# Performance work log

Hardware: AMD Instinct MI355X
Metric: run time of the kernel (lower is better)

The kernel has to match this reference:

```python
import jax, jax.numpy as jnp
import numpy as np

H = 4096        # hidden_size
NH = 32         # num query heads
NG = 8          # num query groups (kv heads)
HD = H // NH    # head size = 128
B, S = 2, 2048


def gen_rope_cache(seq_length, n_elem, base=10000.0):
    theta = 1.0 / base ** (jnp.arange(0, n_elem, 2, dtype=jnp.float32) / n_elem)
    idx_theta = jnp.outer(jnp.arange(seq_length, dtype=jnp.float32), theta)
    return jnp.stack([jnp.cos(idx_theta), jnp.sin(idx_theta)], axis=-1)  # [S, n_elem//2, 2]


def apply_rope(x, cache):
    # x: [B, S, nh, hd], cache: [S, hd//2, 2]; rot_dim == hd (no pass-through)
    b, s, nh, hd = x.shape
    xr = x.reshape(b, s, nh, hd // 2, 2)
    c = cache[:s].reshape(1, s, 1, hd // 2, 2)
    out = jnp.stack([
        xr[..., 0] * c[..., 0] - xr[..., 1] * c[..., 1],
        xr[..., 1] * c[..., 0] + xr[..., 0] * c[..., 1],
    ], axis=-1)
    return out.reshape(b, s, nh, hd)


def setup_inputs() -> dict:
    key = jax.random.key(0)
    k1, k2, k3, k4 = jax.random.split(key, 4)
    x = jax.random.normal(k1, (B, S, H), dtype=jnp.float32)
    W_qkv = jax.random.normal(k2, (H, H + 2 * NG * HD), dtype=jnp.float32) * 0.02
    b_qkv = jax.random.normal(k3, (H + 2 * NG * HD,), dtype=jnp.float32) * 0.02
    W_dense = jax.random.normal(k4, (H, H), dtype=jnp.float32) * 0.02
    rope_cache = gen_rope_cache(S, HD)
    return {"x": x, "rope_cache": rope_cache, "W_qkv": W_qkv, "b_qkv": b_qkv, "W_dense": W_dense}


def reference(x, rope_cache, W_qkv, b_qkv, W_dense):
    b, s, h = x.shape
    qkv = jnp.einsum('bsh,ho->bso', x, W_qkv) + b_qkv
    q, k, v = jnp.split(qkv, [h, h + NG * HD], axis=-1)
    q = q.reshape(b, s, NH, HD)
    k = k.reshape(b, s, NG, HD)
    v = v.reshape(b, s, NG, HD)
    q = apply_rope(q, rope_cache)
    k = apply_rope(k, rope_cache)
    # GQA: group query heads [B, G, rep, S, D] against kv [B, G, S, D]
    rep = NH // NG
    qg = q.transpose(0, 2, 1, 3).reshape(b, NG, rep, s, HD)
    kg = k.transpose(0, 2, 1, 3)  # [B, G, S, D]
    vg = v.transpose(0, 2, 1, 3)
    scale = 1.0 / jnp.sqrt(jnp.float32(HD))
    scores = jnp.einsum('bgrqd,bgkd->bgrqk', qg, kg) * scale
    causal = jnp.tril(jnp.ones((s, s), dtype=bool))
    scores = jnp.where(causal, scores, jnp.float32(-1e30))
    attn = jax.nn.softmax(scores, axis=-1)
    out = jnp.einsum('bgrqk,bgkd->bgrqd', attn, vg)  # [B, G, rep, S, D]
    out = out.reshape(b, NH, s, HD).transpose(0, 2, 1, 3).reshape(b, s, h)
    return jnp.einsum('bsh,ho->bso', out, W_dense)
```

## Files before the change

### kernel.cpp

```cpp
#include <hip/hip_runtime.h>
#include <hip/hip_bf16.h>
#include <math.h>

#define BS   4096
#define HH   4096
#define NH   32
#define NG   8
#define HD   128
#define SEQ  2048
#define NQKV 6144

typedef float f32x4 __attribute__((ext_vector_type(4)));
typedef float f32x16 __attribute__((ext_vector_type(16)));
typedef short s16x8 __attribute__((ext_vector_type(8)));
typedef short s16x4 __attribute__((ext_vector_type(4)));
typedef unsigned int u32x4 __attribute__((ext_vector_type(4)));

__device__ __forceinline__ unsigned short f2bf(float f) {
  unsigned int u = __builtin_bit_cast(unsigned int, f);
  unsigned int r = (u + 0x7fffu + ((u >> 16) & 1u)) >> 16;
  return (unsigned short)r;
}
__device__ __forceinline__ float b2f(short h) {
  unsigned int u = ((unsigned int)(unsigned short)h) << 16;
  return __builtin_bit_cast(float, u);
}

__device__ __forceinline__ void gload16(const void* g, void* l) {
  __builtin_amdgcn_global_load_lds((__attribute__((address_space(1))) void*)(g),
                                   (__attribute__((address_space(3))) void*)(l), 16, 0, 0);
}

#define BARRIER __builtin_amdgcn_s_barrier()
#define PRIO1 __builtin_amdgcn_s_setprio(1)
#define PRIO0 __builtin_amdgcn_s_setprio(0)

__global__ void cast_f32_bf16(const float* __restrict__ in, short* __restrict__ out, long n4) {
  long i = (long)blockIdx.x * blockDim.x + threadIdx.x;
  long stride = (long)gridDim.x * blockDim.x;
  for (; i < n4; i += stride) {
    float4 v = *(const float4*)&in[i * 4];
    s16x4 o;
    o[0] = (short)f2bf(v.x); o[1] = (short)f2bf(v.y);
    o[2] = (short)f2bf(v.z); o[3] = (short)f2bf(v.w);
    *(s16x4*)&out[i * 4] = o;
  }
}

__global__ __launch_bounds__(256) void transpose_cast(const float* __restrict__ in,
                                                      short* __restrict__ out, int R, int C) {
  __shared__ float tile[32][33];
  int tx = threadIdx.x & 31, ty = threadIdx.x >> 5;
  long c0 = (long)blockIdx.x * 32, r0 = (long)blockIdx.y * 32;
#pragma unroll
  for (int j = 0; j < 32; j += 8)
    tile[ty + j][tx] = in[(r0 + ty + j) * C + c0 + tx];
  __syncthreads();
#pragma unroll
  for (int j = 0; j < 32; j += 8)
    out[(c0 + ty + j) * R + r0 + tx] = (short)f2bf(tile[tx][ty + j]);
}

#define LDA_FR(BASE, DB)                                                         \
  {                                                                              \
    _Pragma("unroll") for (int mf = 0; mf < 4; ++mf)                             \
      _Pragma("unroll") for (int ks = 0; ks < 2; ++ks)                           \
        af[mf][ks] = *(const s16x8*)&lds[(BASE) + (DB) * 8192 + aoff[mf][ks]];   \
  }
#define LDB_FR(BASE, DB)                                                         \
  {                                                                              \
    _Pragma("unroll") for (int nf = 0; nf < 2; ++nf)                             \
      _Pragma("unroll") for (int ks = 0; ks < 2; ++ks)                           \
        bf[nf][ks] = *(const s16x8*)&lds[(BASE) + (DB) * 8192 + boff[nf][ks]];   \
  }
#define MF_Q(MS, NS)                                                             \
  {                                                                              \
    _Pragma("unroll") for (int ks = 0; ks < 2; ++ks)                             \
      _Pragma("unroll") for (int mf = 0; mf < 4; ++mf)                           \
        _Pragma("unroll") for (int nf = 0; nf < 2; ++nf)                         \
          acc[(MS) * 4 + mf][(NS) * 2 + nf] = __builtin_amdgcn_mfma_f32_16x16x32_bf16( \
              af[mf][ks], bf[nf][ks], acc[(MS) * 4 + mf][(NS) * 2 + nf], 0, 0, 0);     \
  }
#define STG_AU0(DB, KB) { gload16(sA0 + (KB), &lds[0 + (DB) * 8192 + du0]);            \
                          gload16(sA1 + (KB), &lds[0 + (DB) * 8192 + du1]); }
#define STG_BU0(DB, KB) { gload16(sB0 + (KB), &lds[32768 + (DB) * 8192 + du0]);        \
                          gload16(sB1 + (KB), &lds[32768 + (DB) * 8192 + du1]); }
#define STG_AU1(DB, KB) { gload16(sA0 + 64 * (long)K + (KB), &lds[16384 + (DB) * 8192 + du0]); \
                          gload16(sA1 + 64 * (long)K + (KB), &lds[16384 + (DB) * 8192 + du1]); }
#define STG_BU1(DB, KB) { gload16(sB0 + 32 * (long)K + (KB), &lds[49152 + (DB) * 8192 + du0]); \
                          gload16(sB1 + 32 * (long)K + (KB), &lds[49152 + (DB) * 8192 + du1]); }

#define TILE256(DB, KBS)                                                         \
  LDA_FR(0, DB); LDB_FR(32768, DB);                                              \
  STG_AU0(DB ^ 1, KBS); STG_BU0(DB ^ 1, KBS);                                    \
  BARRIER;                                                                       \
  PRIO1; MF_Q(0, 0); PRIO0;                                                      \
  asm volatile("s_waitcnt vmcnt(6)" ::: "memory");                               \
  BARRIER;                                                                       \
  LDB_FR(49152, DB);                                                             \
  STG_BU1(DB ^ 1, KBS);                                                          \
  BARRIER;                                                                       \
  PRIO1; MF_Q(0, 1); PRIO0;                                                      \
  asm volatile("s_waitcnt vmcnt(6)" ::: "memory");                               \
  BARRIER;                                                                       \
  LDA_FR(16384, DB);                                                             \
  STG_AU1(DB ^ 1, KBS);                                                          \
  BARRIER;                                                                       \
  PRIO1; MF_Q(1, 1); PRIO0;                                                      \
  BARRIER;                                                                       \
  LDB_FR(32768, DB);                                                             \
  BARRIER;                                                                       \
  PRIO1; MF_Q(1, 0); PRIO0;                                                      \
  asm volatile("s_waitcnt vmcnt(4)" ::: "memory");                               \
  BARRIER;

template <int MODE>
__global__ __launch_bounds__(512, 1) void gemm256(const short* __restrict__ A,
                                                  const short* __restrict__ Bt,
                                                  const float* __restrict__ bias,
                                                  void* __restrict__ Cout,
                                                  const float* __restrict__ cache,
                                                  short* __restrict__ Qb,
                                                  short* __restrict__ Kb,
                                                  short* __restrict__ Vtb,
                                                  int M, int N, int K) {
  extern __shared__ short lds[];
  const int t = threadIdx.x;
  const int lane = t & 63, w = t >> 6;
  const int g = lane >> 4, lr = lane & 15;
  const int wm = w >> 2, wn = w & 3;
  const long bm = (long)blockIdx.y * 256;
  const long bn = (long)blockIdx.x * 256;

  const short *sA0, *sA1, *sB0, *sB1;
  {
    int c0 = t, c1 = t + 512;
    int h0 = c0 >> 9, r0 = (c0 >> 3) & 63, tc0 = (c0 & 7) ^ (r0 & 7);
    int h1 = c1 >> 9, r1 = (c1 >> 3) & 63, tc1 = (c1 & 7) ^ (r1 & 7);
    sA0 = A + (bm + h0 * 128 + r0) * (long)K + tc0 * 8;
    sA1 = A + (bm + h1 * 128 + r1) * (long)K + tc1 * 8;
    int g0 = c0 >> 8, rb0 = (c0 >> 3) & 31, tb0 = (c0 & 7) ^ (rb0 & 7);
    int g1 = c1 >> 8, rb1 = (c1 >> 3) & 31, tb1 = (c1 & 7) ^ (rb1 & 7);
    sB0 = Bt + (bn + g0 * 64 + rb0) * (long)K + tb0 * 8;
    sB1 = Bt + (bn + g1 * 64 + rb1) * (long)K + tb1 * 8;
  }
  const int du0 = w * 512;
  const int du1 = w * 512 + 4096;

  int aoff[4][2], boff[2][2];
#pragma unroll
  for (int mf = 0; mf < 4; ++mf)
#pragma unroll
    for (int ks = 0; ks < 2; ++ks)
      aoff[mf][ks] = wm * 4096 + (mf * 16 + lr) * 64 + (((ks * 4 + g) ^ (lr & 7)) * 8);
#pragma unroll
  for (int nf = 0; nf < 2; ++nf)
#pragma unroll
    for (int ks = 0; ks < 2; ++ks)
      boff[nf][ks] = wn * 2048 + (nf * 16 + lr) * 64 + (((ks * 4 + g) ^ (lr & 7)) * 8);

  f32x4 acc[8][4] = {};
  s16x8 af[4][2], bf[2][2];

  STG_AU0(0, 0); STG_BU0(0, 0); STG_AU1(0, 0); STG_BU1(0, 0);
  asm volatile("s_waitcnt vmcnt(0)" ::: "memory");
  BARRIER;

  const int NT = K >> 6;
  for (int kt = 0; kt < NT; kt += 2) {
    const long kb1 = (long)(kt + 1) * 64;
    const long kb2 = (kt + 2 < NT) ? (long)(kt + 2) * 64 : 0l;
    TILE256(0, kb1);
    TILE256(1, kb2);
  }

  if (MODE == 0) {
#pragma unroll
    for (int am = 0; am < 8; ++am) {
      long row = bm + wm * 128 + am * 16 + g * 4;
#pragma unroll
      for (int an = 0; an < 4; ++an) {
        long col = bn + wn * 64 + an * 16 + lr;
#pragma unroll
        for (int r = 0; r < 4; ++r)
          ((float*)Cout)[(row + r) * N + col] = acc[am][an][r];
      }
    }
  } else {
    const float scq = 0.12751743f;
#pragma unroll
    for (int am = 0; am < 8; ++am) {
      int row0 = (int)bm + wm * 128 + am * 16 + g * 4;
      int s0 = row0 & (SEQ - 1);
      int bb = row0 >> 11;
#pragma unroll
      for (int an = 0; an < 4; ++an) {
        int col = (int)bn + wn * 64 + an * 16 + lr;
        float bv = bias[col];
        if (col < HH) {
          int h = col >> 7, d = col & 127;
          const int odd = lr & 1;
#pragma unroll
          for (int r = 0; r < 4; ++r) {
            float v = acc[am][an][r] + bv;
            float p = __shfl_xor(v, 1);
            float2 cs = *(const float2*)&cache[((long)(s0 + r) * 64 + (d >> 1)) * 2];
            float o = odd ? (v * cs.x + p * cs.y) : (v * cs.x - p * cs.y);
            Qb[((long)(bb * NH + h) * SEQ + s0 + r) * HD + d] = (short)f2bf(o * scq);
          }
        } else if (col < HH + NG * HD) {
          int cc = col - HH;
          int gi = cc >> 7, d = cc & 127;
          const int odd = lr & 1;
#pragma unroll
          for (int r = 0; r < 4; ++r) {
            float v = acc[am][an][r] + bv;
            float p = __shfl_xor(v, 1);
            float2 cs = *(const float2*)&cache[((long)(s0 + r) * 64 + (d >> 1)) * 2];
            float o = odd ? (v * cs.x + p * cs.y) : (v * cs.x - p * cs.y);
            Kb[((long)(bb * NG + gi) * SEQ + s0 + r) * HD + d] = (short)f2bf(o);
          }
        } else {
          int cc = col - HH - NG * HD;
          int gi = cc >> 7, d = cc & 127;
          s16x4 o;
#pragma unroll
          for (int r = 0; r < 4; ++r) o[r] = (short)f2bf(acc[am][an][r] + bv);
          *(s16x4*)&Vtb[((long)(bb * NG + gi) * HD + d) * SEQ + s0] = o;
        }
      }
    }
  }
}

__global__ __launch_bounds__(512, 1) void attn(const short* __restrict__ Qb,
                                               const short* __restrict__ Kb,
                                               const short* __restrict__ Vtb,
                                               short* __restrict__ Ob) {
  extern __shared__ short alds[];
  const int t = threadIdx.x, lane = t & 63, w = t >> 6;
  const int l31 = lane & 31, hi = lane >> 5;
  const int qt = 7 - (int)(blockIdx.x >> 6);
  const int head = blockIdx.x & 63;
  const int b = head >> 5, h = head & 31;
  const int qb = qt * 256;
  const short* Qhead = Qb + (long)(b * NH + h) * SEQ * HD;
  const short* Khead = Kb + (long)(b * NG + (h >> 2)) * SEQ * HD;
  const short* Vthead = Vtb + (long)(b * NG + (h >> 2)) * SEQ * HD;
  const int qw0 = qb + w * 32;
  const int qrow = qw0 + l31;
  float* facs = (float*)&alds[32768] + w * 32;

  s16x8 qf[8];
#pragma unroll
  for (int ds = 0; ds < 8; ++ds)
    qf[ds] = *(const s16x8*)&Qhead[(long)qrow * HD + ds * 16 + hi * 8];

  const short *kp0, *kp1, *vp0, *vp1;
  {
    int c0 = t, c1 = t + 512;
    int kr0 = c0 >> 4, kc0 = (c0 & 15) ^ (kr0 & 15);
    int kr1 = c1 >> 4, kc1 = (c1 & 15) ^ (kr1 & 15);
    kp0 = Khead + (long)kr0 * HD + kc0 * 8;
    kp1 = Khead + (long)kr1 * HD + kc1 * 8;
    int vr0 = c0 >> 3, vc0 = (c0 & 7) ^ (vr0 & 7);
    int vr1 = c1 >> 3, vc1 = (c1 & 7) ^ (vr1 & 7);
    vp0 = Vthead + (long)vr0 * SEQ + vc0 * 8;
    vp1 = Vthead + (long)vr1 * SEQ + vc1 * 8;
  }
  const int d0 = w * 512, d1 = w * 512 + 4096;

  f32x16 ao[4] = {};
  float mrun = -1.0e30f, lrun = 0.0f;
  const int nkt = 4 * qt + 4;

  gload16(kp0, &alds[d0]); gload16(kp1, &alds[d1]);
  gload16(vp0, &alds[16384 + d0]); gload16(vp1, &alds[16384 + d1]);
  kp0 += 64 * HD; kp1 += 64 * HD; vp0 += 64; vp1 += 64;
  asm volatile("s_waitcnt vmcnt(0)" ::: "memory");
  BARRIER;

  for (int kt = 0; kt < nkt; ++kt) {
    const int buf = kt & 1, nb = buf ^ 1;
    const int kb = kt * 64;
    const int bK = buf * 8192, bV = 16384 + buf * 8192;
    if (kt + 1 < nkt) {
      gload16(kp0, &alds[nb * 8192 + d0]); gload16(kp1, &alds[nb * 8192 + d1]);
      gload16(vp0, &alds[16384 + nb * 8192 + d0]); gload16(vp1, &alds[16384 + nb * 8192 + d1]);
      kp0 += 64 * HD; kp1 += 64 * HD; vp0 += 64; vp1 += 64;
    }
    if (kb <= qw0 + 31) {
      f32x16 st0 = {}, st1 = {};
      PRIO1;
#pragma unroll
      for (int ds = 0; ds < 8; ++ds) {
        const int c = ds * 2 + hi;
        const int r0 = l31, r1 = 32 + l31;
        s16x8 kf0 = *(const s16x8*)&alds[bK + r0 * 128 + ((c ^ (r0 & 15)) * 8)];
        s16x8 kf1 = *(const s16x8*)&alds[bK + r1 * 128 + ((c ^ (r1 & 15)) * 8)];
        st0 = __builtin_amdgcn_mfma_f32_32x32x16_bf16(kf0, qf[ds], st0, 0, 0, 0);
        st1 = __builtin_amdgcn_mfma_f32_32x32x16_bf16(kf1, qf[ds], st1, 0, 0, 0);
      }
      PRIO0;

      float p[32];
      if (kb + 63 > qrow || kb + 63 > qw0) {
#pragma unroll
        for (int r = 0; r < 16; ++r) {
          int kg = kb + (r & 3) + 8 * (r >> 2) + 4 * hi;
          p[r] = (kg > qrow) ? -1.0e30f : st0[r];
          p[16 + r] = (kg + 32 > qrow) ? -1.0e30f : st1[r];
        }
      } else {
#pragma unroll
        for (int r = 0; r < 16; ++r) { p[r] = st0[r]; p[16 + r] = st1[r]; }
      }
      float tmax = -1.0e30f;
#pragma unroll
      for (int i = 0; i < 32; ++i) tmax = fmaxf(tmax, p[i]);
      tmax = fmaxf(tmax, __shfl_xor(tmax, 32));
      if (!__all(tmax <= mrun + 8.0f)) {
        float mnew = fmaxf(mrun, tmax);
        float fac = exp2f(mrun - mnew);
        facs[l31] = fac;
        mrun = mnew; lrun *= fac;
        f32x4 f0 = *(f32x4*)&facs[0 + 4 * hi];
        f32x4 f1 = *(f32x4*)&facs[8 + 4 * hi];
        f32x4 f2 = *(f32x4*)&facs[16 + 4 * hi];
        f32x4 f3 = *(f32x4*)&facs[24 + 4 * hi];
#pragma unroll
        for (int j = 0; j < 4; ++j)
#pragma unroll
          for (int dt = 0; dt < 4; ++dt) {
            ao[dt][j] *= f0[j]; ao[dt][4 + j] *= f1[j];
            ao[dt][8 + j] *= f2[j]; ao[dt][12 + j] *= f3[j];
          }
      }
      float tsum = 0.0f;
#pragma unroll
      for (int i = 0; i < 32; ++i) { p[i] = exp2f(p[i] - mrun); tsum += p[i]; }
      lrun += tsum + __shfl_xor(tsum, 32);

      s16x8 pa[4];
#pragma unroll
      for (int ks = 0; ks < 4; ++ks) {
        unsigned w0, w1, w2, w3;
        asm("v_cvt_pk_bf16_f32 %0, %1, %2" : "=v"(w0) : "v"(p[ks * 8 + 0]), "v"(p[ks * 8 + 1]));
        asm("v_cvt_pk_bf16_f32 %0, %1, %2" : "=v"(w1) : "v"(p[ks * 8 + 2]), "v"(p[ks * 8 + 3]));
        asm("v_cvt_pk_bf16_f32 %0, %1, %2" : "=v"(w2) : "v"(p[ks * 8 + 4]), "v"(p[ks * 8 + 5]));
        asm("v_cvt_pk_bf16_f32 %0, %1, %2" : "=v"(w3) : "v"(p[ks * 8 + 6]), "v"(p[ks * 8 + 7]));
        unsigned sw0 = (unsigned)__shfl_xor((int)w0, 32);
        unsigned sw1 = (unsigned)__shfl_xor((int)w1, 32);
        unsigned sw2 = (unsigned)__shfl_xor((int)w2, 32);
        unsigned sw3 = (unsigned)__shfl_xor((int)w3, 32);
        u32x4 pw;
        pw[0] = hi ? sw2 : w0;
        pw[1] = hi ? sw3 : w1;
        pw[2] = hi ? w2 : sw0;
        pw[3] = hi ? w3 : sw1;
        pa[ks] = __builtin_bit_cast(s16x8, pw);
      }

      PRIO1;
#pragma unroll
      for (int ks = 0; ks < 4; ++ks)
#pragma unroll
        for (int dt = 0; dt < 4; ++dt) {
          int dd = dt * 32 + l31;
          int slot = (ks * 2 + hi) ^ (dd & 7);
          s16x8 vf = *(const s16x8*)&alds[bV + dd * 64 + slot * 8];
          ao[dt] = __builtin_amdgcn_mfma_f32_32x32x16_bf16(pa[ks], vf, ao[dt], 0, 0, 0);
        }
      PRIO0;
    }
    asm volatile("s_waitcnt vmcnt(0)" ::: "memory");
    BARRIER;
  }

  facs[l31] = 1.0f / lrun;
  float invr[16];
  {
    f32x4 i0 = *(f32x4*)&facs[0 + 4 * hi];
    f32x4 i1 = *(f32x4*)&facs[8 + 4 * hi];
    f32x4 i2 = *(f32x4*)&facs[16 + 4 * hi];
    f32x4 i3 = *(f32x4*)&facs[24 + 4 * hi];
#pragma unroll
    for (int j = 0; j < 4; ++j) {
      invr[j] = i0[j]; invr[4 + j] = i1[j]; invr[8 + j] = i2[j]; invr[12 + j] = i3[j];
    }
  }
#pragma unroll
  for (int dt = 0; dt < 4; ++dt)
#pragma unroll
    for (int r = 0; r < 16; ++r) {
      int grow = qw0 + (r & 3) + 8 * (r >> 2) + 4 * hi;
      Ob[((long)b * SEQ + grow) * HH + h * HD + dt * 32 + l31] = (short)f2bf(ao[dt][r] * invr[r]);
    }
}

extern "C" void kernel_launch(void* const* d_in, const int* in_sizes, int n_in,
                              void* d_out, int out_size, void* d_ws, size_t ws_size,
                              hipStream_t stream) {
  const float* x     = (const float*)d_in[0];
  const float* cache = (const float*)d_in[1];
  const float* Wqkv  = (const float*)d_in[2];
  const float* bqkv  = (const float*)d_in[3];
  const float* Wd    = (const float*)d_in[4];

  char* ws = (char*)d_ws;
  short* xb   = (short*)(ws);
  short* wqt  = (short*)(ws + 33554432ll);
  short* wdt  = (short*)(ws + 83886080ll);
  short* Qb   = (short*)(ws + 167772160ll);
  short* Kb   = (short*)(ws + 201326592ll);
  short* Vtb  = (short*)(ws + 218103808ll);
  short* Ob   = (short*)(ws + 226492416ll);

  cast_f32_bf16<<<2048, 256, 0, stream>>>(x, xb, (long)BS * HH / 4);
  transpose_cast<<<dim3(NQKV / 32, HH / 32), 256, 0, stream>>>(Wqkv, wqt, HH, NQKV);
  transpose_cast<<<dim3(HH / 32, HH / 32), 256, 0, stream>>>(Wd, wdt, HH, HH);
  gemm256<2><<<dim3(NQKV / 256, BS / 256), 512, 131072, stream>>>(
      xb, wqt, bqkv, nullptr, cache, Qb, Kb, Vtb, BS, NQKV, HH);
  attn<<<512, 512, 66560, stream>>>(Qb, Kb, Vtb, Ob);
  gemm256<0><<<dim3(HH / 256, BS / 256), 512, 131072, stream>>>(
      Ob, wdt, nullptr, d_out, nullptr, nullptr, nullptr, nullptr, BS, HH, HH);
}
```

Before: 517.4 us.

## Reorder GEMM inner tile by k-substep with smaller register fragments

```diff
diff --git a/kernel.cpp b/kernel.cpp
--- a/kernel.cpp
+++ b/kernel.cpp
@@ -61,26 +61,18 @@
     out[(c0 + ty + j) * R + r0 + tx] = (short)f2bf(tile[tx][ty + j]);
 }
 
-#define LDA_FR(BASE, DB)                                                         \
-  {                                                                              \
-    _Pragma("unroll") for (int mf = 0; mf < 4; ++mf)                             \
-      _Pragma("unroll") for (int ks = 0; ks < 2; ++ks)                           \
-        af[mf][ks] = *(const s16x8*)&lds[(BASE) + (DB) * 8192 + aoff[mf][ks]];   \
-  }
-#define LDB_FR(BASE, DB)                                                         \
-  {                                                                              \
-    _Pragma("unroll") for (int nf = 0; nf < 2; ++nf)                             \
-      _Pragma("unroll") for (int ks = 0; ks < 2; ++ks)                           \
-        bf[nf][ks] = *(const s16x8*)&lds[(BASE) + (DB) * 8192 + boff[nf][ks]];   \
-  }
-#define MF_Q(MS, NS)                                                             \
-  {                                                                              \
-    _Pragma("unroll") for (int ks = 0; ks < 2; ++ks)                             \
-      _Pragma("unroll") for (int mf = 0; mf < 4; ++mf)                           \
-        _Pragma("unroll") for (int nf = 0; nf < 2; ++nf)                         \
-          acc[(MS) * 4 + mf][(NS) * 2 + nf] = __builtin_amdgcn_mfma_f32_16x16x32_bf16( \
-              af[mf][ks], bf[nf][ks], acc[(MS) * 4 + mf][(NS) * 2 + nf], 0, 0, 0);     \
-  }
+#define LDA4(MSB, DB, KS)                                                        \
+  { _Pragma("unroll") for (int mf = 0; mf < 4; ++mf)                             \
+      af4[mf] = *(const s16x8*)&lds[(MSB) + (DB) * 8192 + aoff[mf][KS]]; }
+#define LDB4(DB, KS)                                                             \
+  { _Pragma("unroll") for (int nf = 0; nf < 2; ++nf) {                           \
+      bfr[nf] = *(const s16x8*)&lds[32768 + (DB) * 8192 + boff[nf][KS]];         \
+      bfr[2 + nf] = *(const s16x8*)&lds[49152 + (DB) * 8192 + boff[nf][KS]]; } }
+#define MF_P(MS)                                                                 \
+  { _Pragma("unroll") for (int mf = 0; mf < 4; ++mf)                             \
+      _Pragma("unroll") for (int j = 0; j < 4; ++j)                              \
+        acc[(MS) * 4 + mf][j] = __builtin_amdgcn_mfma_f32_16x16x32_bf16(         \
+            af4[mf], bfr[j], acc[(MS) * 4 + mf][j], 0, 0, 0); }
 #define STG_AU0(DB, KB) { gload16(sA0 + (KB), &lds[0 + (DB) * 8192 + du0]);            \
                           gload16(sA1 + (KB), &lds[0 + (DB) * 8192 + du1]); }
 #define STG_BU0(DB, KB) { gload16(sB0 + (KB), &lds[32768 + (DB) * 8192 + du0]);        \
@@ -91,27 +83,25 @@
                           gload16(sB1 + 32 * (long)K + (KB), &lds[49152 + (DB) * 8192 + du1]); }
 
 #define TILE256(DB, KBS)                                                         \
-  LDA_FR(0, DB); LDB_FR(32768, DB);                                              \
-  STG_AU0(DB ^ 1, KBS); STG_BU0(DB ^ 1, KBS);                                    \
-  BARRIER;                                                                       \
-  PRIO1; MF_Q(0, 0); PRIO0;                                                      \
+  LDA4(0, DB, 0); LDB4(DB, 0);                                                   \
+  STG_AU0(DB ^ 1, KBS); STG_BU0(DB ^ 1, KBS); STG_BU1(DB ^ 1, KBS);              \
+  BARRIER;                                                                       \
+  PRIO1; MF_P(0); PRIO0;                                                         \
   asm volatile("s_waitcnt vmcnt(6)" ::: "memory");                               \
   BARRIER;                                                                       \
-  LDB_FR(49152, DB);                                                             \
-  STG_BU1(DB ^ 1, KBS);                                                          \
-  BARRIER;                                                                       \
-  PRIO1; MF_Q(0, 1); PRIO0;                                                      \
-  asm volatile("s_waitcnt vmcnt(6)" ::: "memory");                               \
-  BARRIER;                                                                       \
-  LDA_FR(16384, DB);                                                             \
+  LDA4(16384, DB, 0);                                                            \
   STG_AU1(DB ^ 1, KBS);                                                          \
   BARRIER;                                                                       \
-  PRIO1; MF_Q(1, 1); PRIO0;                                                      \
-  BARRIER;                                                                       \
-  LDB_FR(32768, DB);                                                             \
-  BARRIER;                                                                       \
-  PRIO1; MF_Q(1, 0); PRIO0;                                                      \
-  asm volatile("s_waitcnt vmcnt(4)" ::: "memory");                               \
+  PRIO1; MF_P(1); PRIO0;                                                         \
+  BARRIER;                                                                       \
+  LDA4(16384, DB, 1); LDB4(DB, 1);                                               \
+  BARRIER;                                                                       \
+  PRIO1; MF_P(1); PRIO0;                                                         \
+  BARRIER;                                                                       \
+  LDA4(0, DB, 1);                                                                \
+  BARRIER;                                                                       \
+  PRIO1; MF_P(0); PRIO0;                                                         \
+  asm volatile("s_waitcnt vmcnt(2)" ::: "memory");                               \
   BARRIER;
 
 template <int MODE>
@@ -160,7 +150,7 @@
       boff[nf][ks] = wn * 2048 + (nf * 16 + lr) * 64 + (((ks * 4 + g) ^ (lr & 7)) * 8);
 
   f32x4 acc[8][4] = {};
-  s16x8 af[4][2], bf[2][2];
+  s16x8 af4[4], bfr[4];
 
   STG_AU0(0, 0); STG_BU0(0, 0); STG_AU1(0, 0); STG_BU1(0, 0);
   asm volatile("s_waitcnt vmcnt(0)" ::: "memory");
```

Result: slower. 529.8 us (+2.4%).

## Split QKV GEMM into separate Q and KV kernels to balance CU waves

Applied to the files above, without the earlier changes.

```diff
diff --git a/kernel.cpp b/kernel.cpp
--- a/kernel.cpp
+++ b/kernel.cpp
@@ -121,8 +121,6 @@
                                                   void* __restrict__ Cout,
                                                   const float* __restrict__ cache,
                                                   short* __restrict__ Qb,
-                                                  short* __restrict__ Kb,
-                                                  short* __restrict__ Vtb,
                                                   int M, int N, int K) {
   extern __shared__ short lds[];
   const int t = threadIdx.x;
@@ -197,37 +195,144 @@
       for (int an = 0; an < 4; ++an) {
         int col = (int)bn + wn * 64 + an * 16 + lr;
         float bv = bias[col];
-        if (col < HH) {
-          int h = col >> 7, d = col & 127;
-          const int odd = lr & 1;
-#pragma unroll
-          for (int r = 0; r < 4; ++r) {
-            float v = acc[am][an][r] + bv;
-            float p = __shfl_xor(v, 1);
-            float2 cs = *(const float2*)&cache[((long)(s0 + r) * 64 + (d >> 1)) * 2];
-            float o = odd ? (v * cs.x + p * cs.y) : (v * cs.x - p * cs.y);
-            Qb[((long)(bb * NH + h) * SEQ + s0 + r) * HD + d] = (short)f2bf(o * scq);
-          }
-        } else if (col < HH + NG * HD) {
-          int cc = col - HH;
-          int gi = cc >> 7, d = cc & 127;
-          const int odd = lr & 1;
-#pragma unroll
-          for (int r = 0; r < 4; ++r) {
-            float v = acc[am][an][r] + bv;
-            float p = __shfl_xor(v, 1);
-            float2 cs = *(const float2*)&cache[((long)(s0 + r) * 64 + (d >> 1)) * 2];
-            float o = odd ? (v * cs.x + p * cs.y) : (v * cs.x - p * cs.y);
-            Kb[((long)(bb * NG + gi) * SEQ + s0 + r) * HD + d] = (short)f2bf(o);
-          }
-        } else {
-          int cc = col - HH - NG * HD;
-          int gi = cc >> 7, d = cc & 127;
-          s16x4 o;
-#pragma unroll
-          for (int r = 0; r < 4; ++r) o[r] = (short)f2bf(acc[am][an][r] + bv);
-          *(s16x4*)&Vtb[((long)(bb * NG + gi) * HD + d) * SEQ + s0] = o;
+        int h = col >> 7, d = col & 127;
+        const int odd = lr & 1;
+#pragma unroll
+        for (int r = 0; r < 4; ++r) {
+          float v = acc[am][an][r] + bv;
+          float p = __shfl_xor(v, 1);
+          float2 cs = *(const float2*)&cache[((long)(s0 + r) * 64 + (d >> 1)) * 2];
+          float o = odd ? (v * cs.x + p * cs.y) : (v * cs.x - p * cs.y);
+          Qb[((long)(bb * NH + h) * SEQ + s0 + r) * HD + d] = (short)f2bf(o * scq);
         }
+      }
+    }
+  }
+}
+
+#define KV_LDA(MSB, DB, KS)                                                      \
+  { _Pragma("unroll") for (int mf = 0; mf < 4; ++mf)                             \
+      af[mf] = *(const s16x8*)&lds[(MSB) + (DB) * 8192 + aoff[mf][KS]]; }
+#define KV_LDB(DB, KS)                                                           \
+  { _Pragma("unroll") for (int nf = 0; nf < 2; ++nf)                             \
+      bfk[nf] = *(const s16x8*)&lds[32768 + (DB) * 8192 + boff[nf][KS]]; }
+#define KV_MF(MS)                                                                \
+  { _Pragma("unroll") for (int mf = 0; mf < 4; ++mf)                             \
+      _Pragma("unroll") for (int nf = 0; nf < 2; ++nf)                           \
+        acc[(MS) * 4 + mf][nf] = __builtin_amdgcn_mfma_f32_16x16x32_bf16(        \
+            af[mf], bfk[nf], acc[(MS) * 4 + mf][nf], 0, 0, 0); }
+#define KV_SA0(DB, KB) { gload16(sA0 + (KB), &lds[(DB) * 8192 + du0]);                 \
+                         gload16(sA1 + (KB), &lds[(DB) * 8192 + du1]); }
+#define KV_SA1(DB, KB) { gload16(sA0 + 64 * (long)HH + (KB), &lds[16384 + (DB) * 8192 + du0]); \
+                         gload16(sA1 + 64 * (long)HH + (KB), &lds[16384 + (DB) * 8192 + du1]); }
+#define KV_SB(DB, KB)  { gload16(sB0 + (KB), &lds[32768 + (DB) * 8192 + du0]);         \
+                         gload16(sB1 + (KB), &lds[32768 + (DB) * 8192 + du1]); }
+
+#define KVTILE(DB, KBS)                                                          \
+  KV_LDA(0, DB, 0); KV_LDB(DB, 0);                                               \
+  KV_SA0(DB ^ 1, KBS);                                                           \
+  BARRIER;                                                                       \
+  PRIO1; KV_MF(0); PRIO0;                                                        \
+  asm volatile("s_waitcnt vmcnt(2)" ::: "memory");                               \
+  BARRIER;                                                                       \
+  KV_LDA(16384, DB, 0);                                                          \
+  KV_SB(DB ^ 1, KBS);                                                            \
+  BARRIER;                                                                       \
+  PRIO1; KV_MF(1); PRIO0;                                                        \
+  BARRIER;                                                                       \
+  KV_LDA(16384, DB, 1); KV_LDB(DB, 1);                                           \
+  KV_SA1(DB ^ 1, KBS);                                                           \
+  BARRIER;                                                                       \
+  PRIO1; KV_MF(1); PRIO0;                                                        \
+  BARRIER;                                                                       \
+  KV_LDA(0, DB, 1);                                                              \
+  BARRIER;                                                                       \
+  PRIO1; KV_MF(0); PRIO0;                                                        \
+  asm volatile("s_waitcnt vmcnt(2)" ::: "memory");                               \
+  BARRIER;
+
+__global__ __launch_bounds__(512, 1) void gemm_kv(const short* __restrict__ A,
+                                                  const short* __restrict__ Bt,
+                                                  const float* __restrict__ bias,
+                                                  const float* __restrict__ cache,
+                                                  short* __restrict__ Kb,
+                                                  short* __restrict__ Vtb) {
+  extern __shared__ short lds[];
+  const int t = threadIdx.x;
+  const int lane = t & 63, w = t >> 6;
+  const int g = lane >> 4, lr = lane & 15;
+  const int wm = w >> 2, wn = w & 3;
+  const long bm = (long)blockIdx.y * 256;
+  const int bnl = blockIdx.x * 128;
+
+  const short *sA0, *sA1, *sB0, *sB1;
+  {
+    int c0 = t, c1 = t + 512;
+    int h0 = c0 >> 9, r0 = (c0 >> 3) & 63, tc0 = (c0 & 7) ^ (r0 & 7);
+    int h1 = c1 >> 9, r1 = (c1 >> 3) & 63, tc1 = (c1 & 7) ^ (r1 & 7);
+    sA0 = A + (bm + h0 * 128 + r0) * (long)HH + tc0 * 8;
+    sA1 = A + (bm + h1 * 128 + r1) * (long)HH + tc1 * 8;
+    int rb0 = c0 >> 3, tb0 = (c0 & 7) ^ (rb0 & 7);
+    int rb1 = c1 >> 3, tb1 = (c1 & 7) ^ (rb1 & 7);
+    sB0 = Bt + ((long)bnl + rb0) * HH + tb0 * 8;
+    sB1 = Bt + ((long)bnl + rb1) * HH + tb1 * 8;
+  }
+  const int du0 = w * 512;
+  const int du1 = w * 512 + 4096;
+
+  int aoff[4][2], boff[2][2];
+#pragma unroll
+  for (int mf = 0; mf < 4; ++mf)
+#pragma unroll
+    for (int ks = 0; ks < 2; ++ks)
+      aoff[mf][ks] = wm * 4096 + (mf * 16 + lr) * 64 + (((ks * 4 + g) ^ (lr & 7)) * 8);
+#pragma unroll
+  for (int nf = 0; nf < 2; ++nf)
+#pragma unroll
+    for (int ks = 0; ks < 2; ++ks)
+      boff[nf][ks] = wn * 2048 + (nf * 16 + lr) * 64 + (((ks * 4 + g) ^ (lr & 7)) * 8);
+
+  f32x4 acc[8][2] = {};
+  s16x8 af[4], bfk[2];
+
+  KV_SA0(0, 0); KV_SB(0, 0); KV_SA1(0, 0);
+  asm volatile("s_waitcnt vmcnt(0)" ::: "memory");
+  BARRIER;
+
+  for (int kt = 0; kt < 64; kt += 2) {
+    const long kb1 = (long)(kt + 1) * 64;
+    const long kb2 = (kt + 2 < 64) ? (long)(kt + 2) * 64 : 0l;
+    KVTILE(0, kb1);
+    KVTILE(1, kb2);
+  }
+
+#pragma unroll
+  for (int am = 0; am < 8; ++am) {
+    int row0 = (int)bm + wm * 128 + am * 16 + g * 4;
+    int s0 = row0 & (SEQ - 1);
+    int bb = row0 >> 11;
+#pragma unroll
+    for (int an = 0; an < 2; ++an) {
+      int cl = bnl + wn * 32 + an * 16 + lr;
+      float bv = bias[4096 + cl];
+      if (cl < 1024) {
+        int gi = cl >> 7, d = cl & 127;
+        const int odd = lr & 1;
+#pragma unroll
+        for (int r = 0; r < 4; ++r) {
+          float v = acc[am][an][r] + bv;
+          float p = __shfl_xor(v, 1);
+          float2 cs = *(const float2*)&cache[((long)(s0 + r) * 64 + (d >> 1)) * 2];
+          float o = odd ? (v * cs.x + p * cs.y) : (v * cs.x - p * cs.y);
+          Kb[((long)(bb * NG + gi) * SEQ + s0 + r) * HD + d] = (short)f2bf(o);
+        }
+      } else {
+        int cv = cl - 1024;
+        int gi = cv >> 7, d = cv & 127;
+        s16x4 o;
+#pragma unroll
+        for (int r = 0; r < 4; ++r) o[r] = (short)f2bf(acc[am][an][r] + bv);
+        *(s16x4*)&Vtb[((long)(bb * NG + gi) * HD + d) * SEQ + s0] = o;
       }
     }
   }
@@ -419,9 +524,11 @@
   cast_f32_bf16<<<2048, 256, 0, stream>>>(x, xb, (long)BS * HH / 4);
   transpose_cast<<<dim3(NQKV / 32, HH / 32), 256, 0, stream>>>(Wqkv, wqt, HH, NQKV);
   transpose_cast<<<dim3(HH / 32, HH / 32), 256, 0, stream>>>(Wd, wdt, HH, HH);
-  gemm256<2><<<dim3(NQKV / 256, BS / 256), 512, 131072, stream>>>(
-      xb, wqt, bqkv, nullptr, cache, Qb, Kb, Vtb, BS, NQKV, HH);
+  gemm256<2><<<dim3(16, 16), 512, 131072, stream>>>(
+      xb, wqt, bqkv, nullptr, cache, Qb, BS, HH, HH);
+  gemm_kv<<<dim3(16, 16), 512, 98304, stream>>>(
+      xb, wqt + 4096ll * HH, bqkv, cache, Kb, Vtb);
   attn<<<512, 512, 66560, stream>>>(Qb, Kb, Vtb, Ob);
-  gemm256<0><<<dim3(HH / 256, BS / 256), 512, 131072, stream>>>(
-      Ob, wdt, nullptr, d_out, nullptr, nullptr, nullptr, nullptr, BS, HH, HH);
-}
+  gemm256<0><<<dim3(16, 16), 512, 131072, stream>>>(
+      Ob, wdt, nullptr, d_out, nullptr, nullptr, BS, HH, HH);
+}
```

After: 484.4 us. -6.4%, faster.
